# Kernel optimization log

Hardware: AMD Instinct MI355X
Metric: run time of the kernel (lower is better)

The kernel has to match this reference:

```python
import jax, jax.numpy as jnp
import numpy as np

DIM = 768
NUM_HEADS = 12
HEAD_DIM = DIM // NUM_HEADS
SCALE = HEAD_DIM ** -0.5


def setup_inputs() -> dict:
    key = jax.random.key(0)
    ks = jax.random.split(key, 7)
    B, N = 4, 2048
    s = DIM ** -0.5
    return {
        "x": jax.random.normal(ks[0], (B, N, DIM), dtype=jnp.float32),
        "attn_bias": jax.random.normal(ks[1], (1, NUM_HEADS, N, N), dtype=jnp.float32),
        "Wq": jax.random.normal(ks[2], (DIM, DIM), dtype=jnp.float32) * s,
        "Wk": jax.random.normal(ks[3], (DIM, DIM), dtype=jnp.float32) * s,
        "Wv": jax.random.normal(ks[4], (DIM, DIM), dtype=jnp.float32) * s,
        "Wp": jax.random.normal(ks[5], (DIM, DIM), dtype=jnp.float32) * s,
        "bp": jax.random.normal(ks[6], (DIM,), dtype=jnp.float32) * 0.02,
    }


def reference(x, attn_bias, Wq, Wk, Wv, Wp, bp):
    B, N, C = x.shape
    # Linear layers use y = x @ W.T (torch convention); split heads: [B,H,N,D]
    def heads(y):
        return y.reshape(B, N, NUM_HEADS, HEAD_DIM).transpose(0, 2, 1, 3)
    q = heads(x @ Wq.T)
    k = heads(x @ Wk.T)
    v = heads(x @ Wv.T)
    attn = jnp.einsum("bhnd,bhmd->bhnm", q, k) * SCALE + attn_bias
    attn = jax.nn.softmax(attn, axis=-1)
    out = jnp.einsum("bhnm,bhmd->bhnd", attn, v)
    out = out.transpose(0, 2, 1, 3).reshape(B, N, C)
    return out @ Wp.T + bp
```

## Files before the change

### kernel.cpp

```cpp
#include <hip/hip_runtime.h>
#include <hip/hip_bf16.h>

#define NTOK 2048
#define NHEADS 12
#define HDIM 64
#define DIM 768
#define BATCH 4
#define SC2_    0.18033688011112042f
#define LOG2E_  1.4426950408889634f

typedef __attribute__((ext_vector_type(8))) short short8;
typedef __attribute__((ext_vector_type(4))) float f32x4;
typedef __attribute__((ext_vector_type(16))) float f32x16;

__device__ __forceinline__ short f2bf(float f) {
  union { float f; unsigned u; } v; v.f = f;
  unsigned r = v.u + 0x7fffu + ((v.u >> 16) & 1u);
  return (short)(r >> 16);
}

__device__ __forceinline__ f32x4 mfma_bf16(short8 a, short8 b, f32x4 c) {
  return __builtin_amdgcn_mfma_f32_16x16x32_bf16(a, b, c, 0, 0, 0);
}

__device__ __forceinline__ f32x16 mfma32(short8 a, short8 b, f32x16 c) {
  return __builtin_amdgcn_mfma_f32_32x32x16_bf16(a, b, c, 0, 0, 0);
}

__device__ __forceinline__ void gload_lds16(const void* g, void* l) {
  __builtin_amdgcn_global_load_lds((const __attribute__((address_space(1))) void*)g,
                                   (__attribute__((address_space(3))) void*)l, 16, 0, 0);
}

__device__ __forceinline__ float exp2_hw(float x) {
  float r; asm("v_exp_f32 %0, %1" : "=v"(r) : "v"(x)); return r;
}

__device__ __forceinline__ unsigned cvt_pk_bf16(float lo, float hi) {
  unsigned r; asm("v_cvt_pk_bf16_f32 %0, %1, %2" : "=v"(r) : "v"(lo), "v"(hi)); return r;
}

__device__ __forceinline__ int swz(int r) { return (r ^ (r >> 3)) & 7; }

__global__ void cvt_x(const float* __restrict__ src, short* __restrict__ dst) {
  int i = blockIdx.x * 256 + threadIdx.x;
  float4 v = ((const float4*)src)[i];
  short4 o; o.x = f2bf(v.x); o.y = f2bf(v.y); o.z = f2bf(v.z); o.w = f2bf(v.w);
  ((short4*)dst)[i] = o;
}

__global__ void cvt_w(const float* __restrict__ w0, const float* __restrict__ w1,
                      const float* __restrict__ w2, const float* __restrict__ w3,
                      short* __restrict__ d0, short* __restrict__ d1,
                      short* __restrict__ d2, short* __restrict__ d3) {
  int i = blockIdx.x * 256 + threadIdx.x;
  const float* s = blockIdx.y == 0 ? w0 : blockIdx.y == 1 ? w1 : blockIdx.y == 2 ? w2 : w3;
  short* d = blockIdx.y == 0 ? d0 : blockIdx.y == 1 ? d1 : blockIdx.y == 2 ? d2 : d3;
  float4 v = ((const float4*)s)[i];
  short4 o; o.x = f2bf(v.x); o.y = f2bf(v.y); o.z = f2bf(v.z); o.w = f2bf(v.w);
  ((short4*)d)[i] = o;
}

__device__ __forceinline__ void gemm_mainloop(const short* __restrict__ A,
                                              const short* __restrict__ B,
                                              int mbase, int nbase,
                                              short* As, short* Bs,
                                              f32x4 (&acc)[4][4], int lane, int w) {
  int lr = lane & 15, lg = lane >> 4;
  int wr = w >> 1, wc = w & 1;
  for (int kb = 0; kb < DIM; kb += 64) {
    if (kb) __syncthreads();
#pragma unroll
    for (int c = 0; c < 4; ++c) {
      int row = w * 32 + c * 8 + (lane >> 3);
      int sch = (lane & 7) ^ (row & 7);
      gload_lds16(A + (size_t)(mbase + row) * DIM + kb + sch * 8, (char*)As + w * 4096 + c * 1024);
      gload_lds16(B + (size_t)(nbase + row) * DIM + kb + sch * 8, (char*)Bs + w * 4096 + c * 1024);
    }
    __syncthreads();
#pragma unroll
    for (int ks = 0; ks < 2; ++ks) {
      short8 af[4], bf[4];
#pragma unroll
      for (int i = 0; i < 4; ++i) {
        int row = wr * 64 + i * 16 + lr;
        int ch = (ks * 4 + lg) ^ (row & 7);
        af[i] = *(const short8*)(As + row * 64 + ch * 8);
      }
#pragma unroll
      for (int j = 0; j < 4; ++j) {
        int row = wc * 64 + j * 16 + lr;
        int ch = (ks * 4 + lg) ^ (row & 7);
        bf[j] = *(const short8*)(Bs + row * 64 + ch * 8);
      }
#pragma unroll
      for (int i = 0; i < 4; ++i)
#pragma unroll
        for (int j = 0; j < 4; ++j)
          acc[i][j] = mfma_bf16(af[i], bf[j], acc[i][j]);
    }
  }
}

__global__ __launch_bounds__(256, 2) void gemm_qkv(const short* __restrict__ xb,
    const short* __restrict__ wq, const short* __restrict__ wk, const short* __restrict__ wv,
    short* __restrict__ Qh, short* __restrict__ Kh, short* __restrict__ Vt) {
  __shared__ __align__(16) short As[128 * 64];
  __shared__ __align__(16) short Bs[128 * 64];
  int nt = blockIdx.x, mt = blockIdx.y, z = blockIdx.z;
  const short* B = z == 0 ? wq : (z == 1 ? wk : wv);
  int tid = threadIdx.x, lane = tid & 63, w = tid >> 6;
  f32x4 acc[4][4] = {};
  gemm_mainloop(xb, B, mt * 128, nt * 128, As, Bs, acc, lane, w);
  int lr = lane & 15, lg = lane >> 4, wr = w >> 1, wc = w & 1;
  if (z < 2) {
    short* dst = z == 0 ? Qh : Kh;
    float sc = z == 0 ? SC2_ : 1.f;
#pragma unroll
    for (int i = 0; i < 4; ++i)
#pragma unroll
      for (int j = 0; j < 4; ++j) {
        int m = mt * 128 + wr * 64 + i * 16 + lg * 4;
        int n = nt * 128 + wc * 64 + j * 16 + lr;
        int bb = m >> 11, nn = m & 2047, hh = n >> 6, d = n & 63;
        size_t base = (((size_t)bb * NHEADS + hh) * NTOK + nn) * HDIM + d;
#pragma unroll
        for (int r = 0; r < 4; ++r)
          dst[base + (size_t)r * HDIM] = f2bf(acc[i][j][r] * sc);
      }
  } else {
#pragma unroll
    for (int i = 0; i < 4; ++i)
#pragma unroll
      for (int j = 0; j < 4; ++j) {
        int m = mt * 128 + wr * 64 + i * 16 + lg * 4;
        int n = nt * 128 + wc * 64 + j * 16 + lr;
        int bb = m >> 11, nn = m & 2047, hh = n >> 6, d = n & 63;
        short4 pk;
        pk.x = f2bf(acc[i][j][0]); pk.y = f2bf(acc[i][j][1]);
        pk.z = f2bf(acc[i][j][2]); pk.w = f2bf(acc[i][j][3]);
        *(short4*)(Vt + (((size_t)bb * NHEADS + hh) * HDIM + d) * NTOK + nn) = pk;
      }
  }
}

__global__ __launch_bounds__(256, 3) void attn_fused(const short* __restrict__ Qh,
    const short* __restrict__ Kh, const short* __restrict__ Vt,
    const float* __restrict__ bias, short* __restrict__ Ob) {
  __shared__ __align__(16) short Ks[2][32 * 64];
  __shared__ __align__(16) short Vs[2][32 * 64];
  __shared__ __align__(16) float Bsh[2][128 * 32];
  int d0 = blockIdx.x;
  int wg = (d0 & 7) * 96 + (d0 >> 3);
  int b = wg & 3, qb = (wg >> 2) & 15, h = wg >> 6;
  int tid = threadIdx.x, lane = tid & 63, w = tid >> 6;
  int ql = lane & 31, hi = lane >> 5;

  const short* Q = Qh + ((size_t)b * NHEADS + h) * NTOK * HDIM;
  const short* K = Kh + ((size_t)b * NHEADS + h) * NTOK * HDIM;
  const short* V = Vt + ((size_t)b * NHEADS + h) * HDIM * NTOK;
  int qrow = qb * 128 + w * 32 + ql;
  const float* Bg = bias + ((size_t)h * NTOK + qb * 128) * NTOK;

  short8 qf[4];
#pragma unroll
  for (int i = 0; i < 4; ++i)
    qf[i] = *(const short8*)(Q + (size_t)qrow * HDIM + i * 16 + hi * 8);

  short8 onesv;
#pragma unroll
  for (int i = 0; i < 8; ++i) onesv[i] = (short)0x3F80;

  f32x16 oacc0 = {}, oacc1 = {}, sumacc = {};

  int l8 = lane >> 3, s7 = lane & 7;

  int krow = w * 8 + l8;
  const short* Ksrc = K + (size_t)krow * HDIM + (s7 ^ swz(krow)) * 8;
  int vrp = w * 8 + l8;
  int vu = s7 ^ swz(vrp);
  const short* Vsrc = V + (size_t)(vrp * 2 + (vu >> 2)) * NTOK + (vu & 3) * 8;
  int br0 = w * 32 + 0 + l8, br1 = w * 32 + 8 + l8, br2 = w * 32 + 16 + l8, br3 = w * 32 + 24 + l8;
  const float* Bsrc0 = Bg + (size_t)br0 * NTOK + (s7 ^ swz(br0)) * 4;
  const float* Bsrc1 = Bg + (size_t)br1 * NTOK + (s7 ^ swz(br1)) * 4;
  const float* Bsrc2 = Bg + (size_t)br2 * NTOK + (s7 ^ swz(br2)) * 4;
  const float* Bsrc3 = Bg + (size_t)br3 * NTOK + (s7 ^ swz(br3)) * 4;
  char* Kdst = (char*)Ks[0] + w * 1024;
  char* Vdst = (char*)Vs[0] + w * 1024;
  char* Bdst = (char*)Bsh[0] + w * 4096;

  int sq = swz(ql);
  const short* ka0 = Ks[0] + ql * 64 + ((0 + hi) ^ sq) * 8;
  const short* ka1 = Ks[0] + ql * 64 + ((2 + hi) ^ sq) * 8;
  const short* ka2 = Ks[0] + ql * 64 + ((4 + hi) ^ sq) * 8;
  const short* ka3 = Ks[0] + ql * 64 + ((6 + hi) ^ sq) * 8;
  int brow = w * 32 + ql, sb = swz(brow);
  const float* ba0 = Bsh[0] + brow * 32 + ((0 + hi) ^ sb) * 4;
  const float* ba1 = Bsh[0] + brow * 32 + ((2 + hi) ^ sb) * 4;
  const float* ba2 = Bsh[0] + brow * 32 + ((4 + hi) ^ sb) * 4;
  const float* ba3 = Bsh[0] + brow * 32 + ((6 + hi) ^ sb) * 4;
  int rp0 = ql >> 1, rp1 = 16 + (ql >> 1);
  int sv0 = swz(rp0), sv1 = swz(rp1);
  int q4 = (ql & 1) * 4 + hi;
  const short* va00 = Vs[0] + rp0 * 64 + ((q4 + 0) ^ sv0) * 8;
  const short* va01 = Vs[0] + rp1 * 64 + ((q4 + 0) ^ sv1) * 8;
  const short* va10 = Vs[0] + rp0 * 64 + ((q4 + 2) ^ sv0) * 8;
  const short* va11 = Vs[0] + rp1 * 64 + ((q4 + 2) ^ sv1) * 8;

#define STAGE(CUR)                                                            \
  {                                                                           \
    gload_lds16(Ksrc, Kdst + (CUR) * 4096);  Ksrc += 32 * HDIM;               \
    gload_lds16(Vsrc, Vdst + (CUR) * 4096);  Vsrc += 32;                      \
    gload_lds16(Bsrc0, Bdst + (CUR) * 16384);           Bsrc0 += 32;          \
    gload_lds16(Bsrc1, Bdst + (CUR) * 16384 + 1024);    Bsrc1 += 32;          \
    gload_lds16(Bsrc2, Bdst + (CUR) * 16384 + 2048);    Bsrc2 += 32;          \
    gload_lds16(Bsrc3, Bdst + (CUR) * 16384 + 3072);    Bsrc3 += 32;          \
  }

#define BODY(T, CUR)                                                          \
  {                                                                           \
    if ((T) < NTOK / 32 - 1) STAGE((CUR) ^ 1)                                 \
    short8 kf0 = *(const short8*)(ka0 + (CUR) * 2048);                        \
    short8 kf1 = *(const short8*)(ka1 + (CUR) * 2048);                        \
    short8 kf2 = *(const short8*)(ka2 + (CUR) * 2048);                        \
    short8 kf3 = *(const short8*)(ka3 + (CUR) * 2048);                        \
    f32x4 bv0 = *(const f32x4*)(ba0 + (CUR) * 4096);                          \
    f32x4 bv1 = *(const f32x4*)(ba1 + (CUR) * 4096);                          \
    f32x4 bv2 = *(const f32x4*)(ba2 + (CUR) * 4096);                          \
    f32x4 bv3 = *(const f32x4*)(ba3 + (CUR) * 4096);                          \
    short8 vA = *(const short8*)(va00 + (CUR) * 2048);                        \
    short8 vB = *(const short8*)(va01 + (CUR) * 2048);                        \
    short8 vC = *(const short8*)(va10 + (CUR) * 2048);                        \
    short8 vD = *(const short8*)(va11 + (CUR) * 2048);                        \
    f32x16 sacc = {};                                                         \
    __builtin_amdgcn_s_setprio(1);                                            \
    sacc = mfma32(kf0, qf[0], sacc);                                          \
    sacc = mfma32(kf1, qf[1], sacc);                                          \
    sacc = mfma32(kf2, qf[2], sacc);                                          \
    sacc = mfma32(kf3, qf[3], sacc);                                          \
    __builtin_amdgcn_s_setprio(0);                                            \
    float p[16];                                                              \
    _Pragma("unroll")                                                         \
    for (int r = 0; r < 4; ++r) {                                             \
      p[0 + r]  = exp2_hw(fmaf(bv0[r], LOG2E_, sacc[0 + r]));                 \
      p[4 + r]  = exp2_hw(fmaf(bv1[r], LOG2E_, sacc[4 + r]));                 \
      p[8 + r]  = exp2_hw(fmaf(bv2[r], LOG2E_, sacc[8 + r]));                 \
      p[12 + r] = exp2_hw(fmaf(bv3[r], LOG2E_, sacc[12 + r]));                \
    }                                                                         \
    unsigned Wd[4][2];                                                        \
    _Pragma("unroll")                                                         \
    for (int g = 0; g < 4; ++g) {                                             \
      Wd[g][0] = cvt_pk_bf16(p[g * 4], p[g * 4 + 1]);                         \
      Wd[g][1] = cvt_pk_bf16(p[g * 4 + 2], p[g * 4 + 3]);                     \
    }                                                                         \
    _Pragma("unroll")                                                         \
    for (int cc = 0; cc < 2; ++cc) {                                          \
      auto r0 = __builtin_amdgcn_permlane32_swap(Wd[cc * 2][0], Wd[cc * 2 + 1][0], false, false); \
      auto r1 = __builtin_amdgcn_permlane32_swap(Wd[cc * 2][1], Wd[cc * 2 + 1][1], false, false); \
      union { unsigned u[4]; short8 s; } pb;                                  \
      pb.u[0] = r0[0]; pb.u[1] = r1[0]; pb.u[2] = r0[1]; pb.u[3] = r1[1];     \
      __builtin_amdgcn_s_setprio(1);                                          \
      oacc0 = mfma32(cc ? vC : vA, pb.s, oacc0);                              \
      oacc1 = mfma32(cc ? vD : vB, pb.s, oacc1);                              \
      sumacc = mfma32(onesv, pb.s, sumacc);                                   \
      __builtin_amdgcn_s_setprio(0);                                          \
    }                                                                         \
    __syncthreads();                                                          \
  }

  STAGE(0)
  __syncthreads();

  for (int t = 0; t < NTOK / 32; t += 2) {
    BODY(t, 0)
    BODY(t + 1, 1)
  }
#undef BODY
#undef STAGE

  float inv = 1.f / sumacc[0];
  size_t obase = ((size_t)b * NTOK + qrow) * DIM + h * HDIM;
#pragma unroll
  for (int g = 0; g < 4; ++g) {
    unsigned u0 = cvt_pk_bf16(oacc0[g * 4] * inv, oacc0[g * 4 + 1] * inv);
    unsigned u1 = cvt_pk_bf16(oacc0[g * 4 + 2] * inv, oacc0[g * 4 + 3] * inv);
    uint2 pk0; pk0.x = u0; pk0.y = u1;
    *(uint2*)(Ob + obase + g * 8 + hi * 4) = pk0;
    unsigned u2 = cvt_pk_bf16(oacc1[g * 4] * inv, oacc1[g * 4 + 1] * inv);
    unsigned u3 = cvt_pk_bf16(oacc1[g * 4 + 2] * inv, oacc1[g * 4 + 3] * inv);
    uint2 pk1; pk1.x = u2; pk1.y = u3;
    *(uint2*)(Ob + obase + 32 + g * 8 + hi * 4) = pk1;
  }
}

__global__ __launch_bounds__(256, 2) void gemm_proj(const short* __restrict__ Ob,
    const short* __restrict__ wp, const float* __restrict__ bp, float* __restrict__ out) {
  __shared__ __align__(16) short As[128 * 64];
  __shared__ __align__(16) short Bs[128 * 64];
  int nt = blockIdx.x, mt = blockIdx.y;
  int tid = threadIdx.x, lane = tid & 63, w = tid >> 6;
  f32x4 acc[4][4] = {};
  gemm_mainloop(Ob, wp, mt * 128, nt * 128, As, Bs, acc, lane, w);
  int lr = lane & 15, lg = lane >> 4, wr = w >> 1, wc = w & 1;
#pragma unroll
  for (int j = 0; j < 4; ++j) {
    int n = nt * 128 + wc * 64 + j * 16 + lr;
    float bpv = bp[n];
#pragma unroll
    for (int i = 0; i < 4; ++i) {
      int m = mt * 128 + wr * 64 + i * 16 + lg * 4;
#pragma unroll
      for (int r = 0; r < 4; ++r)
        out[(size_t)(m + r) * DIM + n] = acc[i][j][r] + bpv;
    }
  }
}

extern "C" void kernel_launch(void* const* d_in, const int* in_sizes, int n_in,
                              void* d_out, int out_size, void* d_ws, size_t ws_size,
                              hipStream_t stream) {
  const float* x    = (const float*)d_in[0];
  const float* bias = (const float*)d_in[1];
  const float* Wq   = (const float*)d_in[2];
  const float* Wk   = (const float*)d_in[3];
  const float* Wv   = (const float*)d_in[4];
  const float* Wp   = (const float*)d_in[5];
  const float* bp   = (const float*)d_in[6];
  float* out = (float*)d_out;

  char* ws = (char*)d_ws;
  short* xb  = (short*)(ws);
  short* wqb = (short*)(ws + 12582912);
  short* wkb = (short*)(ws + 13762560);
  short* wvb = (short*)(ws + 14942208);
  short* wpb = (short*)(ws + 16121856);
  short* Qh  = (short*)(ws + 17301504);
  short* Kh  = (short*)(ws + 29884416);
  short* Vt  = (short*)(ws + 42467328);
  short* Ob  = (short*)(ws + 55050240);

  cvt_x<<<6144, 256, 0, stream>>>(x, xb);
  cvt_w<<<dim3(576, 4), 256, 0, stream>>>(Wq, Wk, Wv, Wp, wqb, wkb, wvb, wpb);
  gemm_qkv<<<dim3(6, 64, 3), 256, 0, stream>>>(xb, wqb, wkb, wvb, Qh, Kh, Vt);
  attn_fused<<<768, 256, 0, stream>>>(Qh, Kh, Vt, bias, Ob);
  gemm_proj<<<dim3(6, 64), 256, 0, stream>>>(Ob, wpb, bp, out);
}
```

Measured before the change: 196.1 us.

## Split attention KV range in two and combine partial outputs in a new kernel

Splits each attention block's KV range into two halves, giving twice as many workgroups. Each half writes an unnormalized fp32 partial output and a row sum, and a new combine kernel adds the halves, normalizes and writes bf16. The bias tile is now loaded through registers into a single LDS buffer, and the row sum uses scalar adds plus a shuffle instead of an extra MFMA. This targets latency and occupancy (launch bound raised to 4), at the cost of an extra kernel launch and extra fp32 partial traffic. Like the original, it does no max subtraction, relying on the input range.

```diff
diff --git a/kernel.cpp b/kernel.cpp
--- a/kernel.cpp
+++ b/kernel.cpp
@@ -6,6 +6,7 @@
 #define HDIM 64
 #define DIM 768
 #define BATCH 4
+#define NT_SPLIT 32
 #define SC2_    0.18033688011112042f
 #define LOG2E_  1.4426950408889634f
 
@@ -144,17 +145,18 @@
   }
 }
 
-__global__ __launch_bounds__(256, 3) void attn_fused(const short* __restrict__ Qh,
+__global__ __launch_bounds__(256, 4) void attn_fused(const short* __restrict__ Qh,
     const short* __restrict__ Kh, const short* __restrict__ Vt,
-    const float* __restrict__ bias, short* __restrict__ Ob) {
+    const float* __restrict__ bias, float* __restrict__ Pn, float* __restrict__ Dn) {
   __shared__ __align__(16) short Ks[2][32 * 64];
   __shared__ __align__(16) short Vs[2][32 * 64];
-  __shared__ __align__(16) float Bsh[2][128 * 32];
+  __shared__ __align__(16) float Bsh[128 * 32];
   int d0 = blockIdx.x;
-  int wg = (d0 & 7) * 96 + (d0 >> 3);
-  int b = wg & 3, qb = (wg >> 2) & 15, h = wg >> 6;
+  int wg = (d0 & 7) * 192 + (d0 >> 3);
+  int s = wg & 1, b = (wg >> 1) & 3, qb = (wg >> 3) & 15, h = wg >> 7;
   int tid = threadIdx.x, lane = tid & 63, w = tid >> 6;
   int ql = lane & 31, hi = lane >> 5;
+  int kv0 = s * 1024;
 
   const short* Q = Qh + ((size_t)b * NHEADS + h) * NTOK * HDIM;
   const short* K = Kh + ((size_t)b * NHEADS + h) * NTOK * HDIM;
@@ -167,38 +169,33 @@
   for (int i = 0; i < 4; ++i)
     qf[i] = *(const short8*)(Q + (size_t)qrow * HDIM + i * 16 + hi * 8);
 
-  short8 onesv;
-#pragma unroll
-  for (int i = 0; i < 8; ++i) onesv[i] = (short)0x3F80;
-
-  f32x16 oacc0 = {}, oacc1 = {}, sumacc = {};
+  float psum = 0.f;
+  f32x16 oacc0 = {}, oacc1 = {};
 
   int l8 = lane >> 3, s7 = lane & 7;
 
   int krow = w * 8 + l8;
-  const short* Ksrc = K + (size_t)krow * HDIM + (s7 ^ swz(krow)) * 8;
+  const short* Ksrc = K + (size_t)(kv0 + krow) * HDIM + (s7 ^ swz(krow)) * 8;
   int vrp = w * 8 + l8;
   int vu = s7 ^ swz(vrp);
-  const short* Vsrc = V + (size_t)(vrp * 2 + (vu >> 2)) * NTOK + (vu & 3) * 8;
-  int br0 = w * 32 + 0 + l8, br1 = w * 32 + 8 + l8, br2 = w * 32 + 16 + l8, br3 = w * 32 + 24 + l8;
-  const float* Bsrc0 = Bg + (size_t)br0 * NTOK + (s7 ^ swz(br0)) * 4;
-  const float* Bsrc1 = Bg + (size_t)br1 * NTOK + (s7 ^ swz(br1)) * 4;
-  const float* Bsrc2 = Bg + (size_t)br2 * NTOK + (s7 ^ swz(br2)) * 4;
-  const float* Bsrc3 = Bg + (size_t)br3 * NTOK + (s7 ^ swz(br3)) * 4;
+  const short* Vsrc = V + (size_t)(vrp * 2 + (vu >> 2)) * NTOK + kv0 + (vu & 3) * 8;
   char* Kdst = (char*)Ks[0] + w * 1024;
   char* Vdst = (char*)Vs[0] + w * 1024;
-  char* Bdst = (char*)Bsh[0] + w * 4096;
+
+  int brow = w * 32 + ql;
+  const float* Bsrc = Bg + (size_t)brow * NTOK + kv0 + hi * 16;
+  int sbw = swz(brow);
+  float* bwp = Bsh + brow * 32;
+  const float* ba0 = Bsh + brow * 32 + (((0 + hi) ^ sbw) * 4);
+  const float* ba1 = Bsh + brow * 32 + (((2 + hi) ^ sbw) * 4);
+  const float* ba2 = Bsh + brow * 32 + (((4 + hi) ^ sbw) * 4);
+  const float* ba3 = Bsh + brow * 32 + (((6 + hi) ^ sbw) * 4);
 
   int sq = swz(ql);
   const short* ka0 = Ks[0] + ql * 64 + ((0 + hi) ^ sq) * 8;
   const short* ka1 = Ks[0] + ql * 64 + ((2 + hi) ^ sq) * 8;
   const short* ka2 = Ks[0] + ql * 64 + ((4 + hi) ^ sq) * 8;
   const short* ka3 = Ks[0] + ql * 64 + ((6 + hi) ^ sq) * 8;
-  int brow = w * 32 + ql, sb = swz(brow);
-  const float* ba0 = Bsh[0] + brow * 32 + ((0 + hi) ^ sb) * 4;
-  const float* ba1 = Bsh[0] + brow * 32 + ((2 + hi) ^ sb) * 4;
-  const float* ba2 = Bsh[0] + brow * 32 + ((4 + hi) ^ sb) * 4;
-  const float* ba3 = Bsh[0] + brow * 32 + ((6 + hi) ^ sb) * 4;
   int rp0 = ql >> 1, rp1 = 16 + (ql >> 1);
   int sv0 = swz(rp0), sv1 = swz(rp1);
   int q4 = (ql & 1) * 4 + hi;
@@ -207,31 +204,35 @@
   const short* va10 = Vs[0] + rp0 * 64 + ((q4 + 2) ^ sv0) * 8;
   const short* va11 = Vs[0] + rp1 * 64 + ((q4 + 2) ^ sv1) * 8;
 
-#define STAGE(CUR)                                                            \
-  {                                                                           \
-    gload_lds16(Ksrc, Kdst + (CUR) * 4096);  Ksrc += 32 * HDIM;               \
-    gload_lds16(Vsrc, Vdst + (CUR) * 4096);  Vsrc += 32;                      \
-    gload_lds16(Bsrc0, Bdst + (CUR) * 16384);           Bsrc0 += 32;          \
-    gload_lds16(Bsrc1, Bdst + (CUR) * 16384 + 1024);    Bsrc1 += 32;          \
-    gload_lds16(Bsrc2, Bdst + (CUR) * 16384 + 2048);    Bsrc2 += 32;          \
-    gload_lds16(Bsrc3, Bdst + (CUR) * 16384 + 3072);    Bsrc3 += 32;          \
-  }
+  f32x4 bg0 = *(const f32x4*)(Bsrc + 0);
+  f32x4 bg1 = *(const f32x4*)(Bsrc + 4);
+  f32x4 bg2 = *(const f32x4*)(Bsrc + 8);
+  f32x4 bg3 = *(const f32x4*)(Bsrc + 12);
+  Bsrc += 32;
+  gload_lds16(Ksrc, Kdst); Ksrc += 32 * HDIM;
+  gload_lds16(Vsrc, Vdst); Vsrc += 32;
+  *(f32x4*)(bwp + (((hi * 4 + 0) ^ sbw) * 4)) = bg0;
+  *(f32x4*)(bwp + (((hi * 4 + 1) ^ sbw) * 4)) = bg1;
+  *(f32x4*)(bwp + (((hi * 4 + 2) ^ sbw) * 4)) = bg2;
+  *(f32x4*)(bwp + (((hi * 4 + 3) ^ sbw) * 4)) = bg3;
+  __syncthreads();
 
 #define BODY(T, CUR)                                                          \
   {                                                                           \
-    if ((T) < NTOK / 32 - 1) STAGE((CUR) ^ 1)                                 \
+    bool more = (T) < NT_SPLIT - 1;                                           \
+    if (more) {                                                               \
+      bg0 = *(const f32x4*)(Bsrc + 0);                                        \
+      bg1 = *(const f32x4*)(Bsrc + 4);                                        \
+      bg2 = *(const f32x4*)(Bsrc + 8);                                        \
+      bg3 = *(const f32x4*)(Bsrc + 12);                                       \
+      Bsrc += 32;                                                             \
+      gload_lds16(Ksrc, Kdst + ((CUR) ^ 1) * 4096); Ksrc += 32 * HDIM;        \
+      gload_lds16(Vsrc, Vdst + ((CUR) ^ 1) * 4096); Vsrc += 32;               \
+    }                                                                         \
     short8 kf0 = *(const short8*)(ka0 + (CUR) * 2048);                        \
     short8 kf1 = *(const short8*)(ka1 + (CUR) * 2048);                        \
     short8 kf2 = *(const short8*)(ka2 + (CUR) * 2048);                        \
     short8 kf3 = *(const short8*)(ka3 + (CUR) * 2048);                        \
-    f32x4 bv0 = *(const f32x4*)(ba0 + (CUR) * 4096);                          \
-    f32x4 bv1 = *(const f32x4*)(ba1 + (CUR) * 4096);                          \
-    f32x4 bv2 = *(const f32x4*)(ba2 + (CUR) * 4096);                          \
-    f32x4 bv3 = *(const f32x4*)(ba3 + (CUR) * 4096);                          \
-    short8 vA = *(const short8*)(va00 + (CUR) * 2048);                        \
-    short8 vB = *(const short8*)(va01 + (CUR) * 2048);                        \
-    short8 vC = *(const short8*)(va10 + (CUR) * 2048);                        \
-    short8 vD = *(const short8*)(va11 + (CUR) * 2048);                        \
     f32x16 sacc = {};                                                         \
     __builtin_amdgcn_s_setprio(1);                                            \
     sacc = mfma32(kf0, qf[0], sacc);                                          \
@@ -239,6 +240,10 @@
     sacc = mfma32(kf2, qf[2], sacc);                                          \
     sacc = mfma32(kf3, qf[3], sacc);                                          \
     __builtin_amdgcn_s_setprio(0);                                            \
+    f32x4 bv0 = *(const f32x4*)ba0;                                           \
+    f32x4 bv1 = *(const f32x4*)ba1;                                           \
+    f32x4 bv2 = *(const f32x4*)ba2;                                           \
+    f32x4 bv3 = *(const f32x4*)ba3;                                           \
     float p[16];                                                              \
     _Pragma("unroll")                                                         \
     for (int r = 0; r < 4; ++r) {                                             \
@@ -247,12 +252,24 @@
       p[8 + r]  = exp2_hw(fmaf(bv2[r], LOG2E_, sacc[8 + r]));                 \
       p[12 + r] = exp2_hw(fmaf(bv3[r], LOG2E_, sacc[12 + r]));                \
     }                                                                         \
+    psum += ((p[0] + p[1]) + (p[2] + p[3])) + ((p[4] + p[5]) + (p[6] + p[7])) \
+          + ((p[8] + p[9]) + (p[10] + p[11])) + ((p[12] + p[13]) + (p[14] + p[15])); \
     unsigned Wd[4][2];                                                        \
     _Pragma("unroll")                                                         \
     for (int g = 0; g < 4; ++g) {                                             \
       Wd[g][0] = cvt_pk_bf16(p[g * 4], p[g * 4 + 1]);                         \
       Wd[g][1] = cvt_pk_bf16(p[g * 4 + 2], p[g * 4 + 3]);                     \
     }                                                                         \
+    if (more) {                                                               \
+      *(f32x4*)(bwp + (((hi * 4 + 0) ^ sbw) * 4)) = bg0;                      \
+      *(f32x4*)(bwp + (((hi * 4 + 1) ^ sbw) * 4)) = bg1;                      \
+      *(f32x4*)(bwp + (((hi * 4 + 2) ^ sbw) * 4)) = bg2;                      \
+      *(f32x4*)(bwp + (((hi * 4 + 3) ^ sbw) * 4)) = bg3;                      \
+    }                                                                         \
+    short8 vA = *(const short8*)(va00 + (CUR) * 2048);                        \
+    short8 vB = *(const short8*)(va01 + (CUR) * 2048);                        \
+    short8 vC = *(const short8*)(va10 + (CUR) * 2048);                        \
+    short8 vD = *(const short8*)(va11 + (CUR) * 2048);                        \
     _Pragma("unroll")                                                         \
     for (int cc = 0; cc < 2; ++cc) {                                          \
       auto r0 = __builtin_amdgcn_permlane32_swap(Wd[cc * 2][0], Wd[cc * 2 + 1][0], false, false); \
@@ -262,35 +279,45 @@
       __builtin_amdgcn_s_setprio(1);                                          \
       oacc0 = mfma32(cc ? vC : vA, pb.s, oacc0);                              \
       oacc1 = mfma32(cc ? vD : vB, pb.s, oacc1);                              \
-      sumacc = mfma32(onesv, pb.s, sumacc);                                   \
       __builtin_amdgcn_s_setprio(0);                                          \
     }                                                                         \
     __syncthreads();                                                          \
   }
 
-  STAGE(0)
-  __syncthreads();
-
-  for (int t = 0; t < NTOK / 32; t += 2) {
+  for (int t = 0; t < NT_SPLIT; t += 2) {
     BODY(t, 0)
     BODY(t + 1, 1)
   }
 #undef BODY
-#undef STAGE
-
-  float inv = 1.f / sumacc[0];
-  size_t obase = ((size_t)b * NTOK + qrow) * DIM + h * HDIM;
+
+  float fs = psum + __shfl_xor(psum, 32);
+  size_t pbase = ((size_t)(s * 48 + b * 12 + h) * NTOK + qrow) * 64;
 #pragma unroll
   for (int g = 0; g < 4; ++g) {
-    unsigned u0 = cvt_pk_bf16(oacc0[g * 4] * inv, oacc0[g * 4 + 1] * inv);
-    unsigned u1 = cvt_pk_bf16(oacc0[g * 4 + 2] * inv, oacc0[g * 4 + 3] * inv);
-    uint2 pk0; pk0.x = u0; pk0.y = u1;
-    *(uint2*)(Ob + obase + g * 8 + hi * 4) = pk0;
-    unsigned u2 = cvt_pk_bf16(oacc1[g * 4] * inv, oacc1[g * 4 + 1] * inv);
-    unsigned u3 = cvt_pk_bf16(oacc1[g * 4 + 2] * inv, oacc1[g * 4 + 3] * inv);
-    uint2 pk1; pk1.x = u2; pk1.y = u3;
-    *(uint2*)(Ob + obase + 32 + g * 8 + hi * 4) = pk1;
-  }
+    f32x4 t0 = {oacc0[g * 4], oacc0[g * 4 + 1], oacc0[g * 4 + 2], oacc0[g * 4 + 3]};
+    *(f32x4*)(Pn + pbase + g * 8 + hi * 4) = t0;
+    f32x4 t1 = {oacc1[g * 4], oacc1[g * 4 + 1], oacc1[g * 4 + 2], oacc1[g * 4 + 3]};
+    *(f32x4*)(Pn + pbase + 32 + g * 8 + hi * 4) = t1;
+  }
+  if (hi == 0)
+    Dn[(size_t)(s * 48 + b * 12 + h) * NTOK + qrow] = fs;
+}
+
+__global__ void attn_combine(const float* __restrict__ Pn, const float* __restrict__ Dn,
+                             short* __restrict__ Ob) {
+  int idx = blockIdx.x * 256 + threadIdx.x;
+  int d4 = idx & 15, n = (idx >> 4) & 2047, bh = idx >> 15;
+  const size_t PS = (size_t)48 * 2048 * 64;
+  size_t poff = ((size_t)bh * 2048 + n) * 64 + d4 * 4;
+  f32x4 a = *(const f32x4*)(Pn + poff);
+  f32x4 c = *(const f32x4*)(Pn + PS + poff);
+  float den = Dn[(size_t)bh * 2048 + n] + Dn[(size_t)48 * 2048 + (size_t)bh * 2048 + n];
+  float inv = 1.f / den;
+  int b = bh / 12, h = bh - b * 12;
+  unsigned u0 = cvt_pk_bf16((a[0] + c[0]) * inv, (a[1] + c[1]) * inv);
+  unsigned u1 = cvt_pk_bf16((a[2] + c[2]) * inv, (a[3] + c[3]) * inv);
+  uint2 pk; pk.x = u0; pk.y = u1;
+  *(uint2*)(Ob + ((size_t)(b * 2048 + n)) * 768 + h * 64 + d4 * 4) = pk;
 }
 
 __global__ __launch_bounds__(256, 2) void gemm_proj(const short* __restrict__ Ob,
@@ -338,10 +365,13 @@
   short* Kh  = (short*)(ws + 29884416);
   short* Vt  = (short*)(ws + 42467328);
   short* Ob  = (short*)(ws + 55050240);
+  float* Pn  = (float*)(ws + 67633152);
+  float* Dn  = (float*)(ws + 117964800);
 
   cvt_x<<<6144, 256, 0, stream>>>(x, xb);
   cvt_w<<<dim3(576, 4), 256, 0, stream>>>(Wq, Wk, Wv, Wp, wqb, wkb, wvb, wpb);
   gemm_qkv<<<dim3(6, 64, 3), 256, 0, stream>>>(xb, wqb, wkb, wvb, Qh, Kh, Vt);
-  attn_fused<<<768, 256, 0, stream>>>(Qh, Kh, Vt, bias, Ob);
+  attn_fused<<<1536, 256, 0, stream>>>(Qh, Kh, Vt, bias, Pn, Dn);
+  attn_combine<<<6144, 256, 0, stream>>>(Pn, Dn, Ob);
   gemm_proj<<<dim3(6, 64), 256, 0, stream>>>(Ob, wpb, bp, out);
 }
```

After: 348.6 us. 77.8% more time.

## Share attention-bias tile across all four batches in one 1024-thread block

Applied to the files above, without the earlier changes.

The attention kernel now launches one 1024-thread workgroup per (head, query block) instead of one per (batch, head, query block). The 16 waves cover 4 batches × 4 row groups, and all of them share a single LDS copy of the bias tile. Each batch keeps its own K/V buffers. The aim is to read the large fp32 bias from global memory once instead of four times. The cost is fewer blocks (192 against a larger CU count), one block per CU, and block-wide syncs across 16 waves, which may hurt occupancy and latency hiding.

```diff
diff --git a/kernel.cpp b/kernel.cpp
--- a/kernel.cpp
+++ b/kernel.cpp
@@ -144,22 +144,23 @@
   }
 }
 
-__global__ __launch_bounds__(256, 3) void attn_fused(const short* __restrict__ Qh,
+__global__ __launch_bounds__(1024, 1) void attn_fused(const short* __restrict__ Qh,
     const short* __restrict__ Kh, const short* __restrict__ Vt,
     const float* __restrict__ bias, short* __restrict__ Ob) {
-  __shared__ __align__(16) short Ks[2][32 * 64];
-  __shared__ __align__(16) short Vs[2][32 * 64];
+  __shared__ __align__(16) short Ksh[4][2][32 * 64];
+  __shared__ __align__(16) short Vsh[4][2][32 * 64];
   __shared__ __align__(16) float Bsh[2][128 * 32];
   int d0 = blockIdx.x;
-  int wg = (d0 & 7) * 96 + (d0 >> 3);
-  int b = wg & 3, qb = (wg >> 2) & 15, h = wg >> 6;
+  int wg = (d0 & 7) * 24 + (d0 >> 3);
+  int qb = wg & 15, h = wg >> 4;
   int tid = threadIdx.x, lane = tid & 63, w = tid >> 6;
   int ql = lane & 31, hi = lane >> 5;
+  int b = w & 3, rg = w >> 2;
 
   const short* Q = Qh + ((size_t)b * NHEADS + h) * NTOK * HDIM;
   const short* K = Kh + ((size_t)b * NHEADS + h) * NTOK * HDIM;
   const short* V = Vt + ((size_t)b * NHEADS + h) * HDIM * NTOK;
-  int qrow = qb * 128 + w * 32 + ql;
+  int qrow = qb * 128 + rg * 32 + ql;
   const float* Bg = bias + ((size_t)h * NTOK + qb * 128) * NTOK;
 
   short8 qf[4];
@@ -175,47 +176,39 @@
 
   int l8 = lane >> 3, s7 = lane & 7;
 
-  int krow = w * 8 + l8;
+  int krow = rg * 8 + l8;
   const short* Ksrc = K + (size_t)krow * HDIM + (s7 ^ swz(krow)) * 8;
-  int vrp = w * 8 + l8;
+  int vrp = rg * 8 + l8;
   int vu = s7 ^ swz(vrp);
   const short* Vsrc = V + (size_t)(vrp * 2 + (vu >> 2)) * NTOK + (vu & 3) * 8;
-  int br0 = w * 32 + 0 + l8, br1 = w * 32 + 8 + l8, br2 = w * 32 + 16 + l8, br3 = w * 32 + 24 + l8;
-  const float* Bsrc0 = Bg + (size_t)br0 * NTOK + (s7 ^ swz(br0)) * 4;
-  const float* Bsrc1 = Bg + (size_t)br1 * NTOK + (s7 ^ swz(br1)) * 4;
-  const float* Bsrc2 = Bg + (size_t)br2 * NTOK + (s7 ^ swz(br2)) * 4;
-  const float* Bsrc3 = Bg + (size_t)br3 * NTOK + (s7 ^ swz(br3)) * 4;
-  char* Kdst = (char*)Ks[0] + w * 1024;
-  char* Vdst = (char*)Vs[0] + w * 1024;
-  char* Bdst = (char*)Bsh[0] + w * 4096;
+  int bsr = w * 8 + l8;
+  const float* Bsrc = Bg + (size_t)bsr * NTOK + (s7 ^ swz(bsr)) * 4;
+  char* Kdst = (char*)&Ksh[b][0][0] + rg * 1024;
+  char* Vdst = (char*)&Vsh[b][0][0] + rg * 1024;
+  char* Bdst = (char*)&Bsh[0][0] + w * 1024;
 
   int sq = swz(ql);
-  const short* ka0 = Ks[0] + ql * 64 + ((0 + hi) ^ sq) * 8;
-  const short* ka1 = Ks[0] + ql * 64 + ((2 + hi) ^ sq) * 8;
-  const short* ka2 = Ks[0] + ql * 64 + ((4 + hi) ^ sq) * 8;
-  const short* ka3 = Ks[0] + ql * 64 + ((6 + hi) ^ sq) * 8;
-  int brow = w * 32 + ql, sb = swz(brow);
-  const float* ba0 = Bsh[0] + brow * 32 + ((0 + hi) ^ sb) * 4;
-  const float* ba1 = Bsh[0] + brow * 32 + ((2 + hi) ^ sb) * 4;
-  const float* ba2 = Bsh[0] + brow * 32 + ((4 + hi) ^ sb) * 4;
-  const float* ba3 = Bsh[0] + brow * 32 + ((6 + hi) ^ sb) * 4;
+  const short* ka0 = &Ksh[b][0][0] + ql * 64 + ((0 + hi) ^ sq) * 8;
+  const short* ka1 = &Ksh[b][0][0] + ql * 64 + ((2 + hi) ^ sq) * 8;
+  const short* ka2 = &Ksh[b][0][0] + ql * 64 + ((4 + hi) ^ sq) * 8;
+  const short* ka3 = &Ksh[b][0][0] + ql * 64 + ((6 + hi) ^ sq) * 8;
+  int brow = rg * 32 + ql, sb = swz(brow);
+  const float* ba0 = &Bsh[0][0] + brow * 32 + ((0 + hi) ^ sb) * 4;
+  const float* ba1 = &Bsh[0][0] + brow * 32 + ((2 + hi) ^ sb) * 4;
+  const float* ba2 = &Bsh[0][0] + brow * 32 + ((4 + hi) ^ sb) * 4;
+  const float* ba3 = &Bsh[0][0] + brow * 32 + ((6 + hi) ^ sb) * 4;
   int rp0 = ql >> 1, rp1 = 16 + (ql >> 1);
   int sv0 = swz(rp0), sv1 = swz(rp1);
   int q4 = (ql & 1) * 4 + hi;
-  const short* va00 = Vs[0] + rp0 * 64 + ((q4 + 0) ^ sv0) * 8;
-  const short* va01 = Vs[0] + rp1 * 64 + ((q4 + 0) ^ sv1) * 8;
-  const short* va10 = Vs[0] + rp0 * 64 + ((q4 + 2) ^ sv0) * 8;
-  const short* va11 = Vs[0] + rp1 * 64 + ((q4 + 2) ^ sv1) * 8;
-
-#define STAGE(CUR)                                                            \
-  {                                                                           \
-    gload_lds16(Ksrc, Kdst + (CUR) * 4096);  Ksrc += 32 * HDIM;               \
-    gload_lds16(Vsrc, Vdst + (CUR) * 4096);  Vsrc += 32;                      \
-    gload_lds16(Bsrc0, Bdst + (CUR) * 16384);           Bsrc0 += 32;          \
-    gload_lds16(Bsrc1, Bdst + (CUR) * 16384 + 1024);    Bsrc1 += 32;          \
-    gload_lds16(Bsrc2, Bdst + (CUR) * 16384 + 2048);    Bsrc2 += 32;          \
-    gload_lds16(Bsrc3, Bdst + (CUR) * 16384 + 3072);    Bsrc3 += 32;          \
-  }
+  const short* va00 = &Vsh[b][0][0] + rp0 * 64 + ((q4 + 0) ^ sv0) * 8;
+  const short* va01 = &Vsh[b][0][0] + rp1 * 64 + ((q4 + 0) ^ sv1) * 8;
+  const short* va10 = &Vsh[b][0][0] + rp0 * 64 + ((q4 + 2) ^ sv0) * 8;
+  const short* va11 = &Vsh[b][0][0] + rp1 * 64 + ((q4 + 2) ^ sv1) * 8;
+
+#define STAGE(BUF)                                                            \
+  { gload_lds16(Ksrc, Kdst + (BUF) * 4096);  Ksrc += 32 * HDIM;               \
+    gload_lds16(Vsrc, Vdst + (BUF) * 4096);  Vsrc += 32;                      \
+    gload_lds16(Bsrc, Bdst + (BUF) * 16384); Bsrc += 32; }
 
 #define BODY(T, CUR)                                                          \
   {                                                                           \
@@ -257,12 +250,12 @@
     for (int cc = 0; cc < 2; ++cc) {                                          \
       auto r0 = __builtin_amdgcn_permlane32_swap(Wd[cc * 2][0], Wd[cc * 2 + 1][0], false, false); \
       auto r1 = __builtin_amdgcn_permlane32_swap(Wd[cc * 2][1], Wd[cc * 2 + 1][1], false, false); \
-      union { unsigned u[4]; short8 s; } pb;                                  \
+      union { unsigned u[4]; short8 ss; } pb;                                 \
       pb.u[0] = r0[0]; pb.u[1] = r1[0]; pb.u[2] = r0[1]; pb.u[3] = r1[1];     \
       __builtin_amdgcn_s_setprio(1);                                          \
-      oacc0 = mfma32(cc ? vC : vA, pb.s, oacc0);                              \
-      oacc1 = mfma32(cc ? vD : vB, pb.s, oacc1);                              \
-      sumacc = mfma32(onesv, pb.s, sumacc);                                   \
+      oacc0 = mfma32(cc ? vC : vA, pb.ss, oacc0);                             \
+      oacc1 = mfma32(cc ? vD : vB, pb.ss, oacc1);                             \
+      sumacc = mfma32(onesv, pb.ss, sumacc);                                  \
       __builtin_amdgcn_s_setprio(0);                                          \
     }                                                                         \
     __syncthreads();                                                          \
@@ -342,6 +335,6 @@
   cvt_x<<<6144, 256, 0, stream>>>(x, xb);
   cvt_w<<<dim3(576, 4), 256, 0, stream>>>(Wq, Wk, Wv, Wp, wqb, wkb, wvb, wpb);
   gemm_qkv<<<dim3(6, 64, 3), 256, 0, stream>>>(xb, wqb, wkb, wvb, Qh, Kh, Vt);
-  attn_fused<<<768, 256, 0, stream>>>(Qh, Kh, Vt, bias, Ob);
+  attn_fused<<<192, 1024, 0, stream>>>(Qh, Kh, Vt, bias, Ob);
   gemm_proj<<<dim3(6, 64), 256, 0, stream>>>(Ob, wpb, bp, out);
 }
```

Measured after the change: 406.4 us. +107.3%, slower.
